# Kernel optimization log

Hardware: AMD Instinct MI355X
Metric: run time of the kernel (lower is better)

The kernel has to match this reference:

```python
import jax, jax.numpy as jnp
import numpy as np

EMB = 768
HEADS = 12
HD = EMB // HEADS
DFF = 4 * EMB
EPS = 1e-5


def layernorm(x, g, b):
    mu = jnp.mean(x, axis=-1, keepdims=True)
    var = jnp.mean(jnp.square(x - mu), axis=-1, keepdims=True)
    return (x - mu) * jax.lax.rsqrt(var + EPS) * g + b


def setup_inputs() -> dict:
    key = jax.random.key(0)
    ks = jax.random.split(key, 12)
    B, L = 16, 1024
    std = 0.02
    return {
        "x": jax.random.normal(ks[0], (B, L, EMB), jnp.float32),
        "ln1_g": jnp.ones((EMB,), jnp.float32),
        "ln1_b": jnp.zeros((EMB,), jnp.float32),
        "Wq": jax.random.normal(ks[1], (EMB, EMB), jnp.float32) * std,
        "bq": jnp.zeros((EMB,), jnp.float32),
        "Wk": jax.random.normal(ks[2], (EMB, EMB), jnp.float32) * std,
        "bk": jnp.zeros((EMB,), jnp.float32),
        "Wv": jax.random.normal(ks[3], (EMB, EMB), jnp.float32) * std,
        "bv": jnp.zeros((EMB,), jnp.float32),
        "Wo": jax.random.normal(ks[4], (EMB, EMB), jnp.float32) * std,
        "bo": jnp.zeros((EMB,), jnp.float32),
        "ln2_g": jnp.ones((EMB,), jnp.float32),
        "ln2_b": jnp.zeros((EMB,), jnp.float32),
        "W1": jax.random.normal(ks[5], (EMB, DFF), jnp.float32) * std,
        "b1": jnp.zeros((DFF,), jnp.float32),
        "W2": jax.random.normal(ks[6], (DFF, EMB), jnp.float32) * std,
        "b2": jnp.zeros((EMB,), jnp.float32),
    }


def reference(x, ln1_g, ln1_b, Wq, bq, Wk, bk, Wv, bv, Wo, bo,
              ln2_g, ln2_b, W1, b1, W2, b2):
    B, L, D = x.shape
    # --- attention (pre-LN) ---
    h = layernorm(x, ln1_g, ln1_b)
    q = (h @ Wq + bq).reshape(B, L, HEADS, HD)
    k = (h @ Wk + bk).reshape(B, L, HEADS, HD)
    v = (h @ Wv + bv).reshape(B, L, HEADS, HD)
    scores = jnp.einsum("blhd,bmhd->bhlm", q, k) / np.sqrt(HD).astype(np.float32)
    attn = jax.nn.softmax(scores, axis=-1)
    ctx = jnp.einsum("bhlm,bmhd->blhd", attn, v).reshape(B, L, D)
    x = x + ctx @ Wo + bo
    # --- MLP (pre-LN), dropout is identity in eval ---
    h = layernorm(x, ln2_g, ln2_b)
    h = jax.nn.gelu(h @ W1 + b1, approximate=False)  # torch nn.GELU default = exact erf
    x = x + h @ W2 + b2
    return x
```

## Files before the change

kernel.cpp:

```cpp
#include <hip/hip_runtime.h>
#include <hip/hip_bf16.h>
#include <math.h>

#define EMB 768
#define DFF 3072
#define HEADS 12
#define HD 64
#define LSEQ 1024
#define BATCH 16
#define BL (BATCH * LSEQ)
#define QKVD 2304
#define QSCALE 0.1803368801111204f

typedef __attribute__((ext_vector_type(8))) short short8;
typedef __attribute__((ext_vector_type(4))) float floatx4;
typedef unsigned short u16;

__device__ __forceinline__ u16 f2bf(float f) {
  union { float f; unsigned u; } c; c.f = f;
  unsigned u = c.u;
  u += 0x7fffu + ((u >> 16) & 1u);
  return (u16)(u >> 16);
}
__device__ __forceinline__ u16 f2bf_trunc(float f) {
  union { float f; unsigned u; } c; c.f = f;
  return (u16)(c.u >> 16);
}
__device__ __forceinline__ float fast_exp2(float x) {
#if __has_builtin(__builtin_amdgcn_exp2f)
  return __builtin_amdgcn_exp2f(x);
#else
  return exp2f(x);
#endif
}
__device__ __forceinline__ float fast_rcp(float x) {
#if __has_builtin(__builtin_amdgcn_rcpf)
  return __builtin_amdgcn_rcpf(x);
#else
  return 1.0f / x;
#endif
}
__device__ __forceinline__ float gelu_fast(float x) {
  float x2 = x * x;
  float u = x * fmaf(0.10294540f, x2, 2.30211423f);
  u = fminf(fmaxf(u, -30.f), 30.f);
  float t = fast_exp2(u);
  return x * t * fast_rcp(t + 1.0f);
}
__device__ __forceinline__ void async16(const u16* g, u16* l) {
  __builtin_amdgcn_global_load_lds(
      (const __attribute__((address_space(1))) unsigned int*)g,
      (__attribute__((address_space(3))) unsigned int*)l, 16, 0, 0);
}
__device__ __forceinline__ short8 load16(const u16* p) {
  return *reinterpret_cast<const short8*>(p);
}

__global__ __launch_bounds__(256) void ln_kernel(const float* __restrict__ x,
                                                 const float* __restrict__ g,
                                                 const float* __restrict__ b,
                                                 u16* __restrict__ out) {
  int row = blockIdx.x * 4 + (threadIdx.x >> 6);
  int lane = threadIdx.x & 63;
  const float* xr = x + (size_t)row * EMB;
  float v[12];
#pragma unroll
  for (int i = 0; i < 3; i++) {
    float4 t = *reinterpret_cast<const float4*>(xr + i * 256 + lane * 4);
    v[i*4+0] = t.x; v[i*4+1] = t.y; v[i*4+2] = t.z; v[i*4+3] = t.w;
  }
  float s = 0.f, ss = 0.f;
#pragma unroll
  for (int i = 0; i < 12; i++) { s += v[i]; ss += v[i] * v[i]; }
#pragma unroll
  for (int off = 1; off < 64; off <<= 1) {
    s  += __shfl_xor(s, off);
    ss += __shfl_xor(ss, off);
  }
  float mu  = s * (1.f / 768.f);
  float var = ss * (1.f / 768.f) - mu * mu;
  float rs  = rsqrtf(var + 1e-5f);
  u16* orow = out + (size_t)row * EMB;
#pragma unroll
  for (int i = 0; i < 3; i++) {
    int col = i * 256 + lane * 4;
    ushort4 o;
    o.x = f2bf((v[i*4+0] - mu) * rs * g[col+0] + b[col+0]);
    o.y = f2bf((v[i*4+1] - mu) * rs * g[col+1] + b[col+1]);
    o.z = f2bf((v[i*4+2] - mu) * rs * g[col+2] + b[col+2]);
    o.w = f2bf((v[i*4+3] - mu) * rs * g[col+3] + b[col+3]);
    *reinterpret_cast<ushort4*>(orow + col) = o;
  }
}

__global__ void wt_kernel(const float* __restrict__ in, u16* __restrict__ out,
                          int K, int N) {
  __shared__ float t[32][33];
  int x0 = blockIdx.x * 32;
  int y0 = blockIdx.y * 32;
  int tx = threadIdx.x, ty = threadIdx.y;
#pragma unroll
  for (int i = 0; i < 4; i++)
    t[ty + i*8][tx] = in[(size_t)(y0 + ty + i*8) * N + x0 + tx];
  __syncthreads();
#pragma unroll
  for (int i = 0; i < 4; i++)
    out[(size_t)(x0 + ty + i*8) * K + y0 + tx] = f2bf(t[tx][ty + i*8]);
}

__global__ void bias_cat(const float* __restrict__ bq, const float* __restrict__ bk,
                         const float* __restrict__ bv, float* __restrict__ o) {
  int i = blockIdx.x * 256 + threadIdx.x;
  if (i >= QKVD) return;
  o[i] = i < EMB ? bq[i] : (i < 2*EMB ? bk[i - EMB] : bv[i - 2*EMB]);
}

__global__ void vtrans_kernel(const u16* __restrict__ qkv, u16* __restrict__ vt) {
  __shared__ u16 t[32][33];
  int l0 = blockIdx.x * 32;
  int d0 = blockIdx.y * 32;
  int bh = blockIdx.z;
  int b = bh / HEADS, h = bh % HEADS;
  int tx = threadIdx.x, ty = threadIdx.y;
#pragma unroll
  for (int i = 0; i < 4; i++)
    t[ty + i*8][tx] = qkv[(size_t)(b * LSEQ + l0 + ty + i*8) * QKVD + 2*EMB + h * HD + d0 + tx];
  __syncthreads();
#pragma unroll
  for (int i = 0; i < 4; i++)
    vt[(size_t)(bh * HD + d0 + ty + i*8) * LSEQ + l0 + tx] = t[tx][ty + i*8];
}

#define BK 64
__global__ __launch_bounds__(256) void gemm_kernel(
    const u16* __restrict__ A, const u16* __restrict__ Bt,
    const float* __restrict__ bias, const float* __restrict__ res,
    u16* __restrict__ outb, float* __restrict__ outf,
    int M, int N, int K, int mode, float scale, int scale_n) {
  __shared__ u16 As[128 * BK];
  __shared__ u16 Bs[128 * BK];
  int tid = threadIdx.x;
  int lane = tid & 63, wave = tid >> 6;
  int wm = wave & 1, wn = wave >> 1;
  int l16 = lane & 15, lhi = lane >> 4;
  int m0 = blockIdx.x * 128, n0 = blockIdx.y * 128;

  floatx4 acc[4][4];
#pragma unroll
  for (int i = 0; i < 4; i++)
#pragma unroll
    for (int j = 0; j < 4; j++) acc[i][j] = {0.f, 0.f, 0.f, 0.f};

  int rr = lane >> 3;
  int cs = ((lane & 7) ^ rr) * 8;
  const u16* aptr = A + (size_t)(m0 + wave * 32 + rr) * K + cs;
  const u16* bptr = Bt + (size_t)(n0 + wave * 32 + rr) * K + cs;
  u16* asl = As + (wave * 32) * BK;
  u16* bsl = Bs + (wave * 32) * BK;

  int l7 = l16 & 7;
  int oa0 = (wm * 64 + l16) * BK + ((lhi ^ l7) * 8);
  int ob0 = (wn * 64 + l16) * BK + ((lhi ^ l7) * 8);
  int oa1 = oa0 ^ 32;
  int ob1 = ob0 ^ 32;

  for (int k0 = 0; k0 < K; k0 += BK) {
    __syncthreads();
#pragma unroll
    for (int i = 0; i < 4; i++) {
      async16(aptr + (size_t)(i * 8) * K + k0, asl + i * 8 * BK);
      async16(bptr + (size_t)(i * 8) * K + k0, bsl + i * 8 * BK);
    }
    __syncthreads();
#pragma unroll
    for (int kk = 0; kk < 2; kk++) {
      int oA = kk ? oa1 : oa0;
      int oB = kk ? ob1 : ob0;
      short8 af[4], bfr[4];
#pragma unroll
      for (int mt = 0; mt < 4; mt++)
        af[mt] = *reinterpret_cast<const short8*>(&As[oA + mt * 16 * BK]);
#pragma unroll
      for (int nt = 0; nt < 4; nt++)
        bfr[nt] = *reinterpret_cast<const short8*>(&Bs[oB + nt * 16 * BK]);
#pragma unroll
      for (int mt = 0; mt < 4; mt++)
#pragma unroll
        for (int nt = 0; nt < 4; nt++)
          acc[mt][nt] = __builtin_amdgcn_mfma_f32_16x16x32_bf16(af[mt], bfr[nt],
                                                                acc[mt][nt], 0, 0, 0);
    }
  }

#pragma unroll
  for (int mt = 0; mt < 4; mt++) {
#pragma unroll
    for (int nt = 0; nt < 4; nt++) {
      int n = n0 + wn*64 + nt*16 + l16;
      float bv = bias[n];
      float sc = (n < scale_n) ? scale : 1.0f;
#pragma unroll
      for (int r = 0; r < 4; r++) {
        int m = m0 + wm*64 + mt*16 + lhi*4 + r;
        float val = acc[mt][nt][r] + bv;
        if (mode == 2) val = gelu_fast(val);
        if (mode == 1) {
          outf[(size_t)m * N + n] = val + res[(size_t)m * N + n];
        } else {
          outb[(size_t)m * N + n] = f2bf(val * sc);
        }
      }
    }
  }
}

#define PSTRIDE 76
__global__ __launch_bounds__(256) void flash_kernel(
    const u16* __restrict__ qkv, const u16* __restrict__ vt,
    u16* __restrict__ ctx) {
  __shared__ u16 Ps[4][2][16][PSTRIDE];
  int tid = threadIdx.x;
  int lane = tid & 63, w = tid >> 6;
  int l16 = lane & 15, lhi = lane >> 4;

  int i = blockIdx.x;
  int bh = (i & 7) | ((i >> 5) << 3);
  int qb = (i >> 3) & 3;
  int b = bh / HEADS, h = bh % HEADS;
  int q0 = qb * 256 + w * 64;

  const u16* qbase = qkv + (size_t)(b * LSEQ) * QKVD + h * HD;
  const u16* kbase = qbase + EMB;
  const u16* vbase = vt + (size_t)(bh * HD) * LSEQ;

  short8 qf[4][2];
#pragma unroll
  for (int st = 0; st < 4; st++)
#pragma unroll
    for (int kk = 0; kk < 2; kk++)
      qf[st][kk] = load16(qbase + (size_t)(q0 + st*16 + l16) * QKVD + kk*32 + lhi*8);

  floatx4 o[4][4];
#pragma unroll
  for (int st = 0; st < 4; st++)
#pragma unroll
    for (int mt = 0; mt < 4; mt++) o[st][mt] = {0.f, 0.f, 0.f, 0.f};
  float l_i[4] = {0.f, 0.f, 0.f, 0.f};

  for (int kt = 0; kt < LSEQ; kt += 64) {
    short8 kf[4][2], vf[4][2];
#pragma unroll
    for (int mt = 0; mt < 4; mt++)
#pragma unroll
      for (int kk = 0; kk < 2; kk++) {
        kf[mt][kk] = load16(kbase + (size_t)(kt + mt*16 + l16) * QKVD + kk*32 + lhi*8);
        vf[mt][kk] = load16(vbase + (size_t)(mt*16 + l16) * LSEQ + kt + kk*32 + lhi*8);
      }

#pragma unroll
    for (int st = 0; st < 4; st++) {
      u16* pbuf = &Ps[w][st & 1][0][0];
      floatx4 s[4];
#pragma unroll
      for (int mt = 0; mt < 4; mt++) s[mt] = {0.f, 0.f, 0.f, 0.f};
#pragma unroll
      for (int mt = 0; mt < 4; mt++)
#pragma unroll
        for (int kk = 0; kk < 2; kk++)
          s[mt] = __builtin_amdgcn_mfma_f32_16x16x32_bf16(kf[mt][kk], qf[st][kk],
                                                          s[mt], 0, 0, 0);
      float ls = 0.f;
#pragma unroll
      for (int mt = 0; mt < 4; mt++) {
        ushort4 pw;
        float p0 = fast_exp2(s[mt][0]), p1 = fast_exp2(s[mt][1]);
        float p2 = fast_exp2(s[mt][2]), p3 = fast_exp2(s[mt][3]);
        ls += (p0 + p1) + (p2 + p3);
        pw.x = f2bf_trunc(p0); pw.y = f2bf_trunc(p1);
        pw.z = f2bf_trunc(p2); pw.w = f2bf_trunc(p3);
        *reinterpret_cast<ushort4*>(&pbuf[l16 * PSTRIDE + mt*16 + lhi*4]) = pw;
      }
      l_i[st] += ls;
      short8 pf0 = load16(&pbuf[l16 * PSTRIDE + 0*32 + lhi*8]);
      short8 pf1 = load16(&pbuf[l16 * PSTRIDE + 1*32 + lhi*8]);
#pragma unroll
      for (int mt = 0; mt < 4; mt++) {
        o[st][mt] = __builtin_amdgcn_mfma_f32_16x16x32_bf16(vf[mt][0], pf0,
                                                            o[st][mt], 0, 0, 0);
        o[st][mt] = __builtin_amdgcn_mfma_f32_16x16x32_bf16(vf[mt][1], pf1,
                                                            o[st][mt], 0, 0, 0);
      }
    }
  }

#pragma unroll
  for (int st = 0; st < 4; st++) {
    l_i[st] += __shfl_xor(l_i[st], 16);
    l_i[st] += __shfl_xor(l_i[st], 32);
  }

#pragma unroll
  for (int st = 0; st < 4; st++) {
    float inv = fast_rcp(l_i[st]);
    size_t rowbase = (size_t)(b * LSEQ + q0 + st*16 + l16) * EMB + h * HD;
#pragma unroll
    for (int mt = 0; mt < 4; mt++) {
      ushort4 ow;
      ow.x = f2bf(o[st][mt][0] * inv); ow.y = f2bf(o[st][mt][1] * inv);
      ow.z = f2bf(o[st][mt][2] * inv); ow.w = f2bf(o[st][mt][3] * inv);
      *reinterpret_cast<ushort4*>(&ctx[rowbase + mt*16 + lhi*4]) = ow;
    }
  }
}

extern "C" void kernel_launch(void* const* d_in, const int* in_sizes, int n_in,
                              void* d_out, int out_size, void* d_ws, size_t ws_size,
                              hipStream_t stream) {
  const float* x    = (const float*)d_in[0];
  const float* ln1g = (const float*)d_in[1];
  const float* ln1b = (const float*)d_in[2];
  const float* Wq   = (const float*)d_in[3];
  const float* bq   = (const float*)d_in[4];
  const float* Wk   = (const float*)d_in[5];
  const float* bk   = (const float*)d_in[6];
  const float* Wv   = (const float*)d_in[7];
  const float* bv   = (const float*)d_in[8];
  const float* Wo   = (const float*)d_in[9];
  const float* bo   = (const float*)d_in[10];
  const float* ln2g = (const float*)d_in[11];
  const float* ln2b = (const float*)d_in[12];
  const float* W1   = (const float*)d_in[13];
  const float* b1   = (const float*)d_in[14];
  const float* W2   = (const float*)d_in[15];
  const float* b2   = (const float*)d_in[16];

  char* ws = (char*)d_ws;
  u16* qkv_bf = (u16*)(ws);
  u16* vt_bf  = (u16*)(ws + (size_t)75497472);
  u16* h_bf   = (u16*)(ws + (size_t)100663296);
  float* x2   = (float*)(ws + (size_t)125829120);
  u16* m_bf   = (u16*)(ws);
  char* wp = ws + (size_t)176160768;
  u16* wqkv = (u16*)(wp);
  u16* wot  = (u16*)(wp + (size_t)3538944);
  u16* w1t  = (u16*)(wp + (size_t)3538944 + 1179648);
  u16* w2t  = (u16*)(wp + (size_t)3538944 + 1179648 + 4718592);
  float* qkvbias = (float*)(wp + (size_t)3538944 + 1179648 + 2*4718592);

  dim3 b256(256), tb(32, 8);

  wt_kernel<<<dim3(24, 24), tb, 0, stream>>>(Wq, wqkv,               EMB, EMB);
  wt_kernel<<<dim3(24, 24), tb, 0, stream>>>(Wk, wqkv + 768*768,     EMB, EMB);
  wt_kernel<<<dim3(24, 24), tb, 0, stream>>>(Wv, wqkv + 2*768*768,   EMB, EMB);
  wt_kernel<<<dim3(24, 24), tb, 0, stream>>>(Wo, wot, EMB, EMB);
  wt_kernel<<<dim3(96, 24), tb, 0, stream>>>(W1, w1t, EMB, DFF);
  wt_kernel<<<dim3(24, 96), tb, 0, stream>>>(W2, w2t, DFF, EMB);
  bias_cat<<<dim3(9), b256, 0, stream>>>(bq, bk, bv, qkvbias);

  ln_kernel<<<dim3(BL/4), b256, 0, stream>>>(x, ln1g, ln1b, h_bf);

  gemm_kernel<<<dim3(128, 18), b256, 0, stream>>>(h_bf, wqkv, qkvbias, nullptr,
      qkv_bf, nullptr, BL, QKVD, EMB, 0, QSCALE, EMB);

  vtrans_kernel<<<dim3(32, 2, BATCH*HEADS), tb, 0, stream>>>(qkv_bf, vt_bf);

  flash_kernel<<<dim3(768), b256, 0, stream>>>(qkv_bf, vt_bf, h_bf);

  gemm_kernel<<<dim3(128, 6), b256, 0, stream>>>(h_bf, wot, bo, x, nullptr, x2,
      BL, EMB, EMB, 1, 1.0f, 0);

  ln_kernel<<<dim3(BL/4), b256, 0, stream>>>(x2, ln2g, ln2b, h_bf);

  gemm_kernel<<<dim3(128, 24), b256, 0, stream>>>(h_bf, w1t, b1, nullptr, m_bf,
      nullptr, BL, DFF, EMB, 2, 1.0f, 0);

  gemm_kernel<<<dim3(128, 6), b256, 0, stream>>>(m_bf, w2t, b2, x2, nullptr,
      (float*)d_out, BL, EMB, DFF, 1, 1.0f, 0);
}
```

Baseline: 624.3 us.

## Swap MFMA operands for vectorized GEMM epilogue and merge weight-prep launches

```diff
diff --git a/kernel.cpp b/kernel.cpp
--- a/kernel.cpp
+++ b/kernel.cpp
@@ -93,12 +93,36 @@
   }
 }
 
-__global__ void wt_kernel(const float* __restrict__ in, u16* __restrict__ out,
-                          int K, int N) {
+__global__ void prep_kernel(const float* __restrict__ Wq, const float* __restrict__ Wk,
+                            const float* __restrict__ Wv, const float* __restrict__ Wo,
+                            const float* __restrict__ W1, const float* __restrict__ W2,
+                            u16* __restrict__ wqkv, u16* __restrict__ wot,
+                            u16* __restrict__ w1t, u16* __restrict__ w2t,
+                            const float* __restrict__ bq, const float* __restrict__ bk,
+                            const float* __restrict__ bv, float* __restrict__ obias) {
   __shared__ float t[32][33];
-  int x0 = blockIdx.x * 32;
-  int y0 = blockIdx.y * 32;
+  int id = blockIdx.x;
   int tx = threadIdx.x, ty = threadIdx.y;
+  if (id >= 6912) {
+    int i = (id - 6912) * 256 + ty * 32 + tx;
+    if (i < QKVD)
+      obias[i] = i < EMB ? bq[i] : (i < 2*EMB ? bk[i - EMB] : bv[i - 2*EMB]);
+    return;
+  }
+  const float* in; u16* out; int K, N, bx, by;
+  if (id < 2304) {
+    int seg = id / 576, rem = id % 576;
+    bx = rem % 24; by = rem / 24; K = EMB; N = EMB;
+    in = seg == 0 ? Wq : seg == 1 ? Wk : seg == 2 ? Wv : Wo;
+    out = seg == 3 ? wot : wqkv + (size_t)seg * EMB * EMB;
+  } else if (id < 4608) {
+    int rem = id - 2304; bx = rem % 96; by = rem / 96;
+    in = W1; out = w1t; K = EMB; N = DFF;
+  } else {
+    int rem = id - 4608; bx = rem % 24; by = rem / 24;
+    in = W2; out = w2t; K = DFF; N = EMB;
+  }
+  int x0 = bx * 32, y0 = by * 32;
 #pragma unroll
   for (int i = 0; i < 4; i++)
     t[ty + i*8][tx] = in[(size_t)(y0 + ty + i*8) * N + x0 + tx];
@@ -106,13 +130,6 @@
 #pragma unroll
   for (int i = 0; i < 4; i++)
     out[(size_t)(x0 + ty + i*8) * K + y0 + tx] = f2bf(t[tx][ty + i*8]);
-}
-
-__global__ void bias_cat(const float* __restrict__ bq, const float* __restrict__ bk,
-                         const float* __restrict__ bv, float* __restrict__ o) {
-  int i = blockIdx.x * 256 + threadIdx.x;
-  if (i >= QKVD) return;
-  o[i] = i < EMB ? bq[i] : (i < 2*EMB ? bk[i - EMB] : bv[i - 2*EMB]);
 }
 
 __global__ void vtrans_kernel(const u16* __restrict__ qkv, u16* __restrict__ vt) {
@@ -187,28 +204,35 @@
       for (int mt = 0; mt < 4; mt++)
 #pragma unroll
         for (int nt = 0; nt < 4; nt++)
-          acc[mt][nt] = __builtin_amdgcn_mfma_f32_16x16x32_bf16(af[mt], bfr[nt],
+          acc[mt][nt] = __builtin_amdgcn_mfma_f32_16x16x32_bf16(bfr[nt], af[mt],
                                                                 acc[mt][nt], 0, 0, 0);
     }
   }
 
 #pragma unroll
   for (int mt = 0; mt < 4; mt++) {
+    int m = m0 + wm*64 + mt*16 + l16;
 #pragma unroll
     for (int nt = 0; nt < 4; nt++) {
-      int n = n0 + wn*64 + nt*16 + l16;
-      float bv = bias[n];
-      float sc = (n < scale_n) ? scale : 1.0f;
-#pragma unroll
-      for (int r = 0; r < 4; r++) {
-        int m = m0 + wm*64 + mt*16 + lhi*4 + r;
-        float val = acc[mt][nt][r] + bv;
-        if (mode == 2) val = gelu_fast(val);
-        if (mode == 1) {
-          outf[(size_t)m * N + n] = val + res[(size_t)m * N + n];
+      int nbase = n0 + wn*64 + nt*16 + lhi*4;
+      float4 bv = *reinterpret_cast<const float4*>(&bias[nbase]);
+      float v0 = acc[mt][nt][0] + bv.x, v1 = acc[mt][nt][1] + bv.y;
+      float v2 = acc[mt][nt][2] + bv.z, v3 = acc[mt][nt][3] + bv.w;
+      if (mode == 1) {
+        float4 r = *reinterpret_cast<const float4*>(&res[(size_t)m * N + nbase]);
+        float4 o; o.x = v0 + r.x; o.y = v1 + r.y; o.z = v2 + r.z; o.w = v3 + r.w;
+        *reinterpret_cast<float4*>(&outf[(size_t)m * N + nbase]) = o;
+      } else {
+        if (mode == 2) {
+          v0 = gelu_fast(v0); v1 = gelu_fast(v1);
+          v2 = gelu_fast(v2); v3 = gelu_fast(v3);
         } else {
-          outb[(size_t)m * N + n] = f2bf(val * sc);
+          float sc = (nbase < scale_n) ? scale : 1.0f;
+          v0 *= sc; v1 *= sc; v2 *= sc; v3 *= sc;
         }
+        ushort4 o;
+        o.x = f2bf(v0); o.y = f2bf(v1); o.z = f2bf(v2); o.w = f2bf(v3);
+        *reinterpret_cast<ushort4*>(&outb[(size_t)m * N + nbase]) = o;
       }
     }
   }
@@ -349,13 +373,8 @@
 
   dim3 b256(256), tb(32, 8);
 
-  wt_kernel<<<dim3(24, 24), tb, 0, stream>>>(Wq, wqkv,               EMB, EMB);
-  wt_kernel<<<dim3(24, 24), tb, 0, stream>>>(Wk, wqkv + 768*768,     EMB, EMB);
-  wt_kernel<<<dim3(24, 24), tb, 0, stream>>>(Wv, wqkv + 2*768*768,   EMB, EMB);
-  wt_kernel<<<dim3(24, 24), tb, 0, stream>>>(Wo, wot, EMB, EMB);
-  wt_kernel<<<dim3(96, 24), tb, 0, stream>>>(W1, w1t, EMB, DFF);
-  wt_kernel<<<dim3(24, 96), tb, 0, stream>>>(W2, w2t, DFF, EMB);
-  bias_cat<<<dim3(9), b256, 0, stream>>>(bq, bk, bv, qkvbias);
+  prep_kernel<<<dim3(6921), tb, 0, stream>>>(Wq, Wk, Wv, Wo, W1, W2,
+      wqkv, wot, w1t, w2t, bq, bk, bv, qkvbias);
 
   ln_kernel<<<dim3(BL/4), b256, 0, stream>>>(x, ln1g, ln1b, h_bf);
 
```

Measured after the change: 562.1 us. 1.11x faster.
